# Kernel optimization log

Measured on AMD Instinct MI355X. Metric: run time of the kernel, lower is better.

## Reference

```python
import jax, jax.numpy as jnp
import numpy as np
import math

N_EMBD = 1024
NUM_HEADS = 16
HEAD_DIM = N_EMBD // NUM_HEADS


def alibi_slopes(num_heads):
    x = (2 ** 8) ** (1.0 / num_heads)
    return jnp.array([1.0 / x ** (i + 1) for i in range(num_heads)], dtype=jnp.float32)


def setup_inputs() -> dict:
    key = jax.random.key(0)
    k1, k2 = jax.random.split(key)
    x = jax.random.normal(k1, (2, 2048, N_EMBD), dtype=jnp.float32)
    W_kqv = jax.random.normal(k2, (3 * N_EMBD, N_EMBD), dtype=jnp.float32) * (1.0 / math.sqrt(N_EMBD))
    return {"x": x, "W_kqv": W_kqv}


def reference(x, W_kqv):
    B, S, E = x.shape
    H, D = NUM_HEADS, HEAD_DIM
    kqv = jnp.einsum('bse,fe->bsf', x, W_kqv)  # Linear without bias
    k, q, v = jnp.split(kqv, 3, axis=-1)       # chunk order: key, query, value
    # [B, H, S, D]
    q = q.reshape(B, S, H, D).transpose(0, 2, 1, 3)
    k = k.reshape(B, S, H, D).transpose(0, 2, 1, 3)
    v = v.reshape(B, S, H, D).transpose(0, 2, 1, 3)
    # ALiBi bias: slopes[h] * (j - i), shape [H, S, S]
    rel = jnp.arange(S)[None, :] - jnp.arange(S)[:, None]  # [S, S]
    bias = alibi_slopes(H)[:, None, None] * rel.astype(jnp.float32)
    scale = math.sqrt(E)  # NOTE: module scales by sqrt(n_embd), not sqrt(head_dim)
    score = jnp.einsum('bhqd,bhkd->bhqk', q, k) / scale + bias[None]
    causal = jnp.tril(jnp.ones((S, S), dtype=bool))
    score = jnp.where(causal[None, None], score, -jnp.inf)
    attn = jax.nn.softmax(score, axis=-1)
    out = jnp.einsum('bhqk,bhkd->bhqd', attn, v)
    return out.transpose(0, 2, 1, 3).reshape(B, S, E)
```

## Files before the change

### kernel.cpp

```cpp
#include <hip/hip_runtime.h>
#include <hip/hip_bf16.h>
#include <math.h>

#define TOTAL_B 2
#define SEQ 2048
#define EMB 1024
#define NH 16
#define HD 64
#define M_GEMM (TOTAL_B*SEQ)
#define N_GEMM (3*EMB)
#define K_GEMM EMB

typedef __attribute__((ext_vector_type(8))) short short8;
typedef __attribute__((ext_vector_type(4))) float f32x4;
typedef __attribute__((ext_vector_type(4))) unsigned u32x4;

static __device__ __forceinline__ short f2bf(float f) {
  union { float f; unsigned u; } v; v.f = f;
  unsigned r = v.u + 0x7fff + ((v.u >> 16) & 1u);
  return (short)(r >> 16);
}

static __device__ __forceinline__ void gload_lds16(const void* g, void* l) {
  __builtin_amdgcn_global_load_lds(
      (const __attribute__((address_space(1))) void*)(uintptr_t)g,
      (__attribute__((address_space(3))) void*)(uintptr_t)l, 16, 0, 0);
}

static __device__ __forceinline__ float exp2v(float x) {
  float r; asm("v_exp_f32 %0, %1" : "=v"(r) : "v"(x)); return r;
}
static __device__ __forceinline__ unsigned cvtpk(float lo, float hi) {
  unsigned r; asm("v_cvt_pk_bf16_f32 %0, %1, %2" : "=v"(r) : "v"(lo), "v"(hi)); return r;
}
static __device__ __forceinline__ void pl32swap(unsigned &a, unsigned &b) {
  asm("v_permlane32_swap_b32 %0, %1" : "+v"(a), "+v"(b));
}

__global__ void cvt_kernel(const float* __restrict__ x, const float* __restrict__ w,
                           short* __restrict__ xb, short* __restrict__ wb) {
  const long nx = (long)M_GEMM * K_GEMM;
  const long nw = (long)N_GEMM * K_GEMM;
  long i = (long)blockIdx.x * blockDim.x + threadIdx.x;
  const long tot = (nx + nw) / 8;
  if (i >= tot) return;
  long e = i * 8;
  const float* s; short* d;
  if (e < nx) { s = x + e; d = xb + e; }
  else        { s = w + (e - nx); d = wb + (e - nx); }
  float4 a = ((const float4*)s)[0];
  float4 b = ((const float4*)s)[1];
  short8 o;
  o[0]=f2bf(a.x); o[1]=f2bf(a.y); o[2]=f2bf(a.z); o[3]=f2bf(a.w);
  o[4]=f2bf(b.x); o[5]=f2bf(b.y); o[6]=f2bf(b.z); o[7]=f2bf(b.w);
  *(short8*)d = o;
}

__global__ __launch_bounds__(256) void qkv_gemm(const short* __restrict__ A, const short* __restrict__ Bm,
                                                short* __restrict__ Kb, short* __restrict__ Qb,
                                                short* __restrict__ Vb) {
  __shared__ __align__(16) short As[128*64];
  __shared__ __align__(16) short Bs[128*64];
  const int tid = threadIdx.x;
  const int lane = tid & 63, wid = tid >> 6;
  const int lr = lane & 15, lg = lane >> 4;
  const int m0 = blockIdx.y * 128, n0 = blockIdx.x * 128;
  const int wm = (wid >> 1) * 64, wn = (wid & 1) * 64;

  f32x4 acc[4][4] = {};

  for (int kt = 0; kt < K_GEMM/64; ++kt) {
#pragma unroll
    for (int i = 0; i < 4; ++i) {
      const int e16 = i*256 + tid;
      const int row = e16 >> 3;
      const int ch  = e16 & 7;
      const int sch = ch ^ (row & 7);
      const short* ga = A  + (size_t)(m0 + row)*K_GEMM + kt*64 + sch*8;
      gload_lds16(ga, As + i*2048 + wid*512);
      const short* gb = Bm + (size_t)(n0 + row)*K_GEMM + kt*64 + sch*8;
      gload_lds16(gb, Bs + i*2048 + wid*512);
    }
    __syncthreads();
#pragma unroll
    for (int kk = 0; kk < 2; ++kk) {
      short8 af[4], bfr[4];
#pragma unroll
      for (int mi = 0; mi < 4; ++mi) {
        const int r = wm + mi*16 + lr;
        const int c = (kk*4 + lg) ^ (r & 7);
        af[mi] = *(const short8*)(As + r*64 + c*8);
      }
#pragma unroll
      for (int ni = 0; ni < 4; ++ni) {
        const int r = wn + ni*16 + lr;
        const int c = (kk*4 + lg) ^ (r & 7);
        bfr[ni] = *(const short8*)(Bs + r*64 + c*8);
      }
#pragma unroll
      for (int mi = 0; mi < 4; ++mi)
#pragma unroll
        for (int ni = 0; ni < 4; ++ni)
          acc[mi][ni] = __builtin_amdgcn_mfma_f32_16x16x32_bf16(af[mi], bfr[ni], acc[mi][ni], 0, 0, 0);
    }
    __syncthreads();
  }

#pragma unroll
  for (int mi = 0; mi < 4; ++mi) {
#pragma unroll
    for (int ni = 0; ni < 4; ++ni) {
#pragma unroll
      for (int r = 0; r < 4; ++r) {
        const int m = m0 + wm + mi*16 + lg*4 + r;
        const int f = n0 + wn + ni*16 + lr;
        const int b = m >> 11, s = m & 2047;
        const int which = f >> 10, fl = f & 1023;
        const int h = fl >> 6, d = fl & 63;
        short* dst = (which == 0) ? Kb : (which == 1) ? Qb : Vb;
        float val = acc[mi][ni][r];
        if (which == 1) val *= 0.04508422f;
        dst[((size_t)((b*NH + h)*SEQ + s))*HD + d] = f2bf(val);
      }
    }
  }
}

__global__ void vtrans(const short* __restrict__ Vb, short* __restrict__ Vt) {
  __shared__ short t[64][72];
  const int hb = blockIdx.y;
  const int s0 = blockIdx.x * 64;
  const short* src = Vb + ((size_t)hb*SEQ + s0)*HD;
  short* dst = Vt + (size_t)hb*HD*SEQ;
  const int tid = threadIdx.x;
#pragma unroll
  for (int i = 0; i < 2; ++i) {
    const int e = i*2048 + tid*8;
    const int r = e >> 6, c = e & 63;
    short8 v = *(const short8*)(src + (size_t)r*HD + c);
#pragma unroll
    for (int j = 0; j < 8; ++j) t[r][c+j] = v[j];
  }
  __syncthreads();
#pragma unroll
  for (int i = 0; i < 2; ++i) {
    const int e = i*2048 + tid*8;
    const int d = e >> 6, ss = e & 63;
    short8 v;
#pragma unroll
    for (int j = 0; j < 8; ++j) v[j] = t[ss+j][d];
    *(short8*)(dst + (size_t)d*SEQ + s0 + ss) = v;
  }
}

__global__ __launch_bounds__(256, 4) void attn_kernel(const short* __restrict__ Kb, const short* __restrict__ Qb,
                                                      const short* __restrict__ Vt, float* __restrict__ Out) {
  __shared__ __align__(16) short Ks[3][64*64];
  __shared__ __align__(16) short Vs[2][64*64];
  const int tid = threadIdx.x, lane = tid & 63, wid = tid >> 6;
  const int lr = lane & 15, lg = lane >> 4;
  const int bh = blockIdx.x;
  const int b = bh >> 4, h = bh & 15;
  const int qt = 31 - blockIdx.y;
  const float slope = exp2f(-0.5f * (float)(h + 1)) * 1.44269504f;
  const short* Kp = Kb + (size_t)bh * SEQ * HD;
  const short* Qp = Qb + (size_t)bh * SEQ * HD;
  const short* Vp = Vt + (size_t)bh * HD * SEQ;
  float* Ob = Out + (size_t)b * SEQ * EMB + (size_t)h * HD;

  const int q0 = qt * 64, qrb = q0 + wid * 16;
  const int nt = qt + 1;

  short8 qf[2];
#pragma unroll
  for (int kk = 0; kk < 2; ++kk)
    qf[kk] = *(const short8*)(Qp + (size_t)(qrb + lr)*HD + kk*32 + lg*8);

  const int bp = ((lr & 4) << 1) | ((lr & 2) << 1) | ((lr & 8) >> 2) | (lr & 1);
  const int cbase = qrb + lr - ((lg & 1) * 8 + (lg >> 1) * 2);

  float m_run = -INFINITY, l_run = 0.f;
  f32x4 o[4] = {};

  auto stageK = [&](int buf, int t) {
    const int kv0 = t * 64;
#pragma unroll
    for (int i = 0; i < 2; ++i) {
      const int e16 = i*256 + tid;
      const int row = e16 >> 3, ch = e16 & 7;
      const int sch = ch ^ (row & 7);
      gload_lds16(Kp + (size_t)(kv0 + row)*HD + sch*8, &Ks[buf][i*2048 + wid*512]);
    }
  };
  auto stageV = [&](int buf, int t) {
    const int kv0 = t * 64;
#pragma unroll
    for (int i = 0; i < 2; ++i) {
      const int e16 = i*256 + tid;
      const int row = e16 >> 3, ch = e16 & 7;
      const int sch = ch ^ (row & 7);
      gload_lds16(Vp + (size_t)row*SEQ + kv0 + sch*8, &Vs[buf][i*2048 + wid*512]);
    }
  };
  auto qkt = [&](int buf, f32x4* sc) {
    short8 kf[4][2];
#pragma unroll
    for (int kvf = 0; kvf < 4; ++kvf) {
      const int row = kvf*16 + bp;
#pragma unroll
      for (int kk = 0; kk < 2; ++kk) {
        const int c = (kk*4 + lg) ^ (row & 7);
        kf[kvf][kk] = *(const short8*)(&Ks[buf][row*64 + c*8]);
      }
    }
    __builtin_amdgcn_s_setprio(1);
#pragma unroll
    for (int kvf = 0; kvf < 4; ++kvf) {
      f32x4 s = {};
      s = __builtin_amdgcn_mfma_f32_16x16x32_bf16(kf[kvf][0], qf[0], s, 0, 0, 0);
      s = __builtin_amdgcn_mfma_f32_16x16x32_bf16(kf[kvf][1], qf[1], s, 0, 0, 0);
      sc[kvf] = s;
    }
    __builtin_amdgcn_s_setprio(0);
  };

  stageK(0, 0);
  if (nt > 1) stageK(1, 1);
  stageV(0, 0);
  __syncthreads();
  f32x4 sc_cur[4], sc_next[4];
  qkt(0, sc_cur);

  int k1 = 1, k2 = 2;
#pragma unroll 1
  for (int t = 0; t < nt; ++t) {
    const int kv0 = t * 64;
    if (t + 2 < nt) stageK(k2, t + 2);
    if (t + 1 < nt) stageV((t + 1) & 1, t + 1);
    if (t + 1 < nt) qkt(k1, sc_next);

    const float dbase = (float)(kv0 - cbase);
    float v[4][4];
    if (t == nt - 1) {
#pragma unroll
      for (int kvf = 0; kvf < 4; ++kvf)
#pragma unroll
        for (int r = 0; r < 4; ++r) {
          const float C = (float)(kvf*16 + (r>>1)*4 + (r&1));
          const float toff = dbase + C;
          float val = fmaf(slope, toff, sc_cur[kvf][r]);
          if (toff > 0.f) val = -INFINITY;
          v[kvf][r] = val;
        }
    } else {
#pragma unroll
      for (int kvf = 0; kvf < 4; ++kvf)
#pragma unroll
        for (int r = 0; r < 4; ++r) {
          const float C = (float)(kvf*16 + (r>>1)*4 + (r&1));
          v[kvf][r] = fmaf(slope, dbase + C, sc_cur[kvf][r]);
        }
    }
    float q0m = fmaxf(fmaxf(v[0][0], v[0][1]), fmaxf(v[0][2], v[0][3]));
    float q1m = fmaxf(fmaxf(v[1][0], v[1][1]), fmaxf(v[1][2], v[1][3]));
    float q2m = fmaxf(fmaxf(v[2][0], v[2][1]), fmaxf(v[2][2], v[2][3]));
    float q3m = fmaxf(fmaxf(v[3][0], v[3][1]), fmaxf(v[3][2], v[3][3]));
    float mt = fmaxf(fmaxf(q0m, q1m), fmaxf(q2m, q3m));
    mt = fmaxf(mt, __shfl_xor(mt, 16, 64));
    mt = fmaxf(mt, __shfl_xor(mt, 32, 64));

    if (__any(mt > m_run + 10.f)) {
      const float mn = fmaxf(m_run, mt);
      const float corr = exp2v(m_run - mn);
      m_run = mn;
      l_run *= corr;
      float co[4];
#pragma unroll
      for (int r = 0; r < 4; ++r) co[r] = __shfl(corr, lg*4 + r, 64);
#pragma unroll
      for (int dt = 0; dt < 4; ++dt)
#pragma unroll
        for (int r = 0; r < 4; ++r) o[dt][r] *= co[r];
    }
#pragma unroll
    for (int kvf = 0; kvf < 4; ++kvf)
#pragma unroll
      for (int r = 0; r < 4; ++r)
        v[kvf][r] = exp2v(v[kvf][r] - m_run);
    float s0 = (v[0][0]+v[0][1]) + (v[0][2]+v[0][3]);
    float s1 = (v[1][0]+v[1][1]) + (v[1][2]+v[1][3]);
    float s2 = (v[2][0]+v[2][1]) + (v[2][2]+v[2][3]);
    float s3 = (v[3][0]+v[3][1]) + (v[3][2]+v[3][3]);
    float lt = (s0+s1) + (s2+s3);
    lt += __shfl_xor(lt, 16, 64);
    lt += __shfl_xor(lt, 32, 64);
    l_run += lt;

    unsigned pk[4][2];
#pragma unroll
    for (int kvf = 0; kvf < 4; ++kvf) {
      pk[kvf][0] = cvtpk(v[kvf][0], v[kvf][1]);
      pk[kvf][1] = cvtpk(v[kvf][2], v[kvf][3]);
    }
    __builtin_amdgcn_s_setprio(1);
#pragma unroll
    for (int ks = 0; ks < 2; ++ks) {
      unsigned w0 = pk[2*ks][0], w1 = pk[2*ks+1][0];
      pl32swap(w0, w1);
      unsigned w2 = pk[2*ks][1], w3 = pk[2*ks+1][1];
      pl32swap(w2, w3);
      u32x4 wv = {w0, w1, w2, w3};
      const short8 pf = __builtin_bit_cast(short8, wv);
#pragma unroll
      for (int dt = 0; dt < 4; ++dt) {
        const int rv = dt*16 + lr;
        const int cv = (ks*4 + lg) ^ (rv & 7);
        const short8 vf = *(const short8*)(&Vs[t & 1][rv*64 + cv*8]);
        o[dt] = __builtin_amdgcn_mfma_f32_16x16x32_bf16(pf, vf, o[dt], 0, 0, 0);
      }
    }
    __builtin_amdgcn_s_setprio(0);

    __syncthreads();
#pragma unroll
    for (int kvf = 0; kvf < 4; ++kvf) sc_cur[kvf] = sc_next[kvf];
    k1 = k2; k2 = (k2 == 2) ? 0 : k2 + 1;
  }

  const float inv = 1.f / l_run;
  float li[4];
#pragma unroll
  for (int r = 0; r < 4; ++r) li[r] = __shfl(inv, lg*4 + r, 64);
#pragma unroll
  for (int dt = 0; dt < 4; ++dt)
#pragma unroll
    for (int r = 0; r < 4; ++r) {
      const int iq = qrb + lg*4 + r;
      Ob[(size_t)iq*EMB + dt*16 + lr] = o[dt][r] * li[r];
    }
}

extern "C" void kernel_launch(void* const* d_in, const int* in_sizes, int n_in,
                              void* d_out, int out_size, void* d_ws, size_t ws_size,
                              hipStream_t stream) {
  const float* x = (const float*)d_in[0];
  const float* w = (const float*)d_in[1];
  char* ws = (char*)d_ws;
  if (ws_size < 39845888u) return;
  short* xb = (short*)(ws);
  short* wb = (short*)(ws + 8388608u);
  short* Kb = (short*)(ws + 14680064u);
  short* Qb = (short*)(ws + 23068672u);
  short* Vb = (short*)(ws + 31457280u);
  short* Vt = xb;
  float* out = (float*)d_out;

  cvt_kernel<<<3584, 256, 0, stream>>>(x, w, xb, wb);
  qkv_gemm<<<dim3(N_GEMM/128, M_GEMM/128), 256, 0, stream>>>(xb, wb, Kb, Qb, Vb);
  vtrans<<<dim3(SEQ/64, TOTAL_B*NH), 256, 0, stream>>>(Vb, Vt);
  attn_kernel<<<dim3(TOTAL_B*NH, 32), 256, 0, stream>>>(Kb, Qb, Vt, out);
}
```

Before: 100.4 us.

## Rework QKV GEMM into 256x192 double-buffered tile with interleaved prefetch

Rewrites the QKV projection GEMM to use 512-thread blocks computing 256x192 output tiles. Shared memory is double-buffered, and the next K-slice is staged in four chunks interleaved between MFMA phases, using explicit barriers, waitcnts and setprio. The aim is to hide global-to-LDS load latency behind matrix math and to raise arithmetic intensity per block. In exchange, each block uses a large LDS footprint, which limits blocks per CU, and the grid shrinks to 256 blocks, roughly one per CU, so there is little slack for load imbalance.

New measurement: 92.76 us. -7.6%, faster.

```diff
diff --git a/kernel.cpp b/kernel.cpp
--- a/kernel.cpp
+++ b/kernel.cpp
@@ -56,73 +56,157 @@
   *(short8*)d = o;
 }
 
-__global__ __launch_bounds__(256) void qkv_gemm(const short* __restrict__ A, const short* __restrict__ Bm,
-                                                short* __restrict__ Kb, short* __restrict__ Qb,
-                                                short* __restrict__ Vb) {
-  __shared__ __align__(16) short As[128*64];
-  __shared__ __align__(16) short Bs[128*64];
+__global__ __launch_bounds__(512, 2) void qkv_gemm(const short* __restrict__ A, const short* __restrict__ Bm,
+                                                   short* __restrict__ Kb, short* __restrict__ Qb,
+                                                   short* __restrict__ Vb) {
+  __shared__ __align__(16) short lds[57344];
   const int tid = threadIdx.x;
-  const int lane = tid & 63, wid = tid >> 6;
+  const int lane = tid & 63;
+  const int wid = tid >> 6;
   const int lr = lane & 15, lg = lane >> 4;
-  const int m0 = blockIdx.y * 128, n0 = blockIdx.x * 128;
-  const int wm = (wid >> 1) * 64, wn = (wid & 1) * 64;
-
-  f32x4 acc[4][4] = {};
-
-  for (int kt = 0; kt < K_GEMM/64; ++kt) {
-#pragma unroll
-    for (int i = 0; i < 4; ++i) {
-      const int e16 = i*256 + tid;
-      const int row = e16 >> 3;
-      const int ch  = e16 & 7;
-      const int sch = ch ^ (row & 7);
-      const short* ga = A  + (size_t)(m0 + row)*K_GEMM + kt*64 + sch*8;
-      gload_lds16(ga, As + i*2048 + wid*512);
-      const short* gb = Bm + (size_t)(n0 + row)*K_GEMM + kt*64 + sch*8;
-      gload_lds16(gb, Bs + i*2048 + wid*512);
-    }
-    __syncthreads();
+  const int m0 = blockIdx.y * 256, n0 = blockIdx.x * 192;
+  const int wr = wid >> 1;
+  const int wc = wid & 1;
+  const int srcRow = tid >> 3;
+  const int srcCh  = (tid & 7) ^ (srcRow & 7);
+
+  f32x4 acc[4][6] = {};
+
+  auto stageA = [&](int buf, int kt, int u) {
+    const int row = u*64 + srcRow;
+    gload_lds16(A + (size_t)(m0 + row)*K_GEMM + kt*64 + srcCh*8,
+                &lds[buf*16384 + u*4096 + tid*8]);
+  };
+  auto stageB = [&](int buf, int kt, int u) {
+    const int row = u*64 + srcRow;
+    gload_lds16(Bm + (size_t)(n0 + row)*K_GEMM + kt*64 + srcCh*8,
+                &lds[32768 + buf*12288 + u*4096 + tid*8]);
+  };
+  auto readA = [&](int buf, int mi, int kk) -> short8 {
+    const int r = wr*64 + mi*16 + lr;
+    const int c = (kk*4 + lg) ^ (r & 7);
+    return *(const short8*)(&lds[buf*16384 + r*64 + c*8]);
+  };
+  auto readB = [&](int buf, int nj, int kk) -> short8 {
+    const int r = wc*96 + nj*16 + lr;
+    const int c = (kk*4 + lg) ^ (r & 7);
+    return *(const short8*)(&lds[32768 + buf*12288 + r*64 + c*8]);
+  };
+
+#pragma unroll
+  for (int u = 0; u < 4; ++u) stageA(0, 0, u);
+#pragma unroll
+  for (int u = 0; u < 3; ++u) stageB(0, 0, u);
+  asm volatile("s_waitcnt vmcnt(0)" ::: "memory");
+  __builtin_amdgcn_s_barrier();
+
+  short8 aq[2][2], bq[6][2];
+  const int NT = K_GEMM / 64;
+#pragma unroll 1
+  for (int kt = 0; kt < NT; ++kt) {
+    const int buf = kt & 1, nb = buf ^ 1;
+    const bool more = (kt + 1 < NT);
+
 #pragma unroll
     for (int kk = 0; kk < 2; ++kk) {
-      short8 af[4], bfr[4];
-#pragma unroll
-      for (int mi = 0; mi < 4; ++mi) {
-        const int r = wm + mi*16 + lr;
-        const int c = (kk*4 + lg) ^ (r & 7);
-        af[mi] = *(const short8*)(As + r*64 + c*8);
+      aq[0][kk] = readA(buf, 0, kk); aq[1][kk] = readA(buf, 1, kk);
+      bq[0][kk] = readB(buf, 0, kk); bq[1][kk] = readB(buf, 1, kk); bq[2][kk] = readB(buf, 2, kk);
+    }
+    if (more) { stageA(nb, kt+1, 0); stageA(nb, kt+1, 1); }
+    __builtin_amdgcn_s_barrier();
+    asm volatile("s_waitcnt lgkmcnt(0)" ::: "memory");
+    __builtin_amdgcn_sched_barrier(0);
+    __builtin_amdgcn_s_setprio(1);
+#pragma unroll
+    for (int mi = 0; mi < 2; ++mi)
+#pragma unroll
+      for (int nj = 0; nj < 3; ++nj)
+#pragma unroll
+        for (int kk = 0; kk < 2; ++kk)
+          acc[mi][nj] = __builtin_amdgcn_mfma_f32_16x16x32_bf16(aq[mi][kk], bq[nj][kk], acc[mi][nj], 0, 0, 0);
+    __builtin_amdgcn_s_setprio(0);
+    __builtin_amdgcn_sched_barrier(0);
+    __builtin_amdgcn_s_barrier();
+
+#pragma unroll
+    for (int kk = 0; kk < 2; ++kk) {
+      bq[3][kk] = readB(buf, 3, kk); bq[4][kk] = readB(buf, 4, kk); bq[5][kk] = readB(buf, 5, kk);
+    }
+    if (more) { stageA(nb, kt+1, 2); stageA(nb, kt+1, 3); }
+    __builtin_amdgcn_s_barrier();
+    asm volatile("s_waitcnt lgkmcnt(0)" ::: "memory");
+    __builtin_amdgcn_sched_barrier(0);
+    __builtin_amdgcn_s_setprio(1);
+#pragma unroll
+    for (int mi = 0; mi < 2; ++mi)
+#pragma unroll
+      for (int nj = 3; nj < 6; ++nj)
+#pragma unroll
+        for (int kk = 0; kk < 2; ++kk)
+          acc[mi][nj] = __builtin_amdgcn_mfma_f32_16x16x32_bf16(aq[mi][kk], bq[nj][kk], acc[mi][nj], 0, 0, 0);
+    __builtin_amdgcn_s_setprio(0);
+    __builtin_amdgcn_sched_barrier(0);
+    __builtin_amdgcn_s_barrier();
+
+#pragma unroll
+    for (int kk = 0; kk < 2; ++kk) {
+      aq[0][kk] = readA(buf, 2, kk); aq[1][kk] = readA(buf, 3, kk);
+    }
+    if (more) { stageB(nb, kt+1, 0); stageB(nb, kt+1, 1); }
+    __builtin_amdgcn_s_barrier();
+    asm volatile("s_waitcnt lgkmcnt(0)" ::: "memory");
+    __builtin_amdgcn_sched_barrier(0);
+    __builtin_amdgcn_s_setprio(1);
+#pragma unroll
+    for (int mi = 0; mi < 2; ++mi)
+#pragma unroll
+      for (int nj = 3; nj < 6; ++nj)
+#pragma unroll
+        for (int kk = 0; kk < 2; ++kk)
+          acc[mi+2][nj] = __builtin_amdgcn_mfma_f32_16x16x32_bf16(aq[mi][kk], bq[nj][kk], acc[mi+2][nj], 0, 0, 0);
+    __builtin_amdgcn_s_setprio(0);
+    __builtin_amdgcn_sched_barrier(0);
+    __builtin_amdgcn_s_barrier();
+
+#pragma unroll
+    for (int kk = 0; kk < 2; ++kk) {
+      bq[0][kk] = readB(buf, 0, kk); bq[1][kk] = readB(buf, 1, kk); bq[2][kk] = readB(buf, 2, kk);
+    }
+    if (more) { stageB(nb, kt+1, 2); }
+    __builtin_amdgcn_s_barrier();
+    asm volatile("s_waitcnt lgkmcnt(0)" ::: "memory");
+    __builtin_amdgcn_sched_barrier(0);
+    __builtin_amdgcn_s_setprio(1);
+#pragma unroll
+    for (int mi = 0; mi < 2; ++mi)
+#pragma unroll
+      for (int nj = 0; nj < 3; ++nj)
+#pragma unroll
+        for (int kk = 0; kk < 2; ++kk)
+          acc[mi+2][nj] = __builtin_amdgcn_mfma_f32_16x16x32_bf16(aq[mi][kk], bq[nj][kk], acc[mi+2][nj], 0, 0, 0);
+    __builtin_amdgcn_s_setprio(0);
+    __builtin_amdgcn_sched_barrier(0);
+
+    asm volatile("s_waitcnt vmcnt(0)" ::: "memory");
+    __builtin_amdgcn_s_barrier();
+  }
+
+#pragma unroll
+  for (int nj = 0; nj < 6; ++nj) {
+    const int f = n0 + wc*96 + nj*16 + lr;
+    const int which = f >> 10, fl = f & 1023;
+    const int h = fl >> 6, d = fl & 63;
+    short* dst = (which == 0) ? Kb : (which == 1) ? Qb : Vb;
+    const float scale = (which == 1) ? 0.04508422f : 1.0f;
+    short* base = dst + (size_t)h*SEQ*HD + d;
+#pragma unroll
+    for (int mi = 0; mi < 4; ++mi)
+#pragma unroll
+      for (int r = 0; r < 4; ++r) {
+        const int m = m0 + wr*64 + mi*16 + lg*4 + r;
+        const int b = m >> 11, s = m & 2047;
+        base[((size_t)b*NH*SEQ + s)*HD] = f2bf(acc[mi][nj][r] * scale);
       }
-#pragma unroll
-      for (int ni = 0; ni < 4; ++ni) {
-        const int r = wn + ni*16 + lr;
-        const int c = (kk*4 + lg) ^ (r & 7);
-        bfr[ni] = *(const short8*)(Bs + r*64 + c*8);
-      }
-#pragma unroll
-      for (int mi = 0; mi < 4; ++mi)
-#pragma unroll
-        for (int ni = 0; ni < 4; ++ni)
-          acc[mi][ni] = __builtin_amdgcn_mfma_f32_16x16x32_bf16(af[mi], bfr[ni], acc[mi][ni], 0, 0, 0);
-    }
-    __syncthreads();
-  }
-
-#pragma unroll
-  for (int mi = 0; mi < 4; ++mi) {
-#pragma unroll
-    for (int ni = 0; ni < 4; ++ni) {
-#pragma unroll
-      for (int r = 0; r < 4; ++r) {
-        const int m = m0 + wm + mi*16 + lg*4 + r;
-        const int f = n0 + wn + ni*16 + lr;
-        const int b = m >> 11, s = m & 2047;
-        const int which = f >> 10, fl = f & 1023;
-        const int h = fl >> 6, d = fl & 63;
-        short* dst = (which == 0) ? Kb : (which == 1) ? Qb : Vb;
-        float val = acc[mi][ni][r];
-        if (which == 1) val *= 0.04508422f;
-        dst[((size_t)((b*NH + h)*SEQ + s))*HD + d] = f2bf(val);
-      }
-    }
   }
 }
 
@@ -356,7 +440,7 @@
   float* out = (float*)d_out;
 
   cvt_kernel<<<3584, 256, 0, stream>>>(x, w, xb, wb);
-  qkv_gemm<<<dim3(N_GEMM/128, M_GEMM/128), 256, 0, stream>>>(xb, wb, Kb, Qb, Vb);
+  qkv_gemm<<<dim3(N_GEMM/192, M_GEMM/256), 512, 0, stream>>>(xb, wb, Kb, Qb, Vb);
   vtrans<<<dim3(SEQ/64, TOTAL_B*NH), 256, 0, stream>>>(Vb, Vt);
   attn_kernel<<<dim3(TOTAL_B*NH, 32), 256, 0, stream>>>(Kb, Qb, Vt, out);
 }
```
